# Optimization experiments

Hardware: AMD Instinct MI355X
Metric: run time of the kernel (lower is better)

Reference implementation:

```python
import jax, jax.numpy as jnp
import numpy as np

INPUT_DIM = 1024
EMBED_DIMS = 128


def setup_inputs() -> dict:
    key = jax.random.key(0)
    ks = jax.random.split(key, 7)
    s_in = 1.0 / np.sqrt(INPUT_DIM)
    x = jax.random.normal(ks[0], (4, 4096, INPUT_DIM), dtype=jnp.float32)
    Wq = jax.random.uniform(ks[1], (INPUT_DIM, EMBED_DIMS), jnp.float32, -s_in, s_in)
    bq = jax.random.uniform(ks[2], (EMBED_DIMS,), jnp.float32, -s_in, s_in)
    Wk = jax.random.uniform(ks[3], (INPUT_DIM, EMBED_DIMS), jnp.float32, -s_in, s_in)
    bk = jax.random.uniform(ks[4], (EMBED_DIMS,), jnp.float32, -s_in, s_in)
    Wv = jax.random.uniform(ks[5], (INPUT_DIM, EMBED_DIMS), jnp.float32, -s_in, s_in)
    bv = jax.random.uniform(ks[6], (EMBED_DIMS,), jnp.float32, -s_in, s_in)
    return {"x": x, "Wq": Wq, "bq": bq, "Wk": Wk, "bk": bk, "Wv": Wv, "bv": bv}


def reference(x, Wq, bq, Wk, bk, Wv, bv):
    # x: [B, L, C]
    Q = jnp.einsum('blc,cd->bld', x, Wq) + bq  # [B, L, D]
    K = jnp.einsum('blc,cd->bld', x, Wk) + bk
    V = jnp.einsum('blc,cd->bld', x, Wv) + bv
    d_k = Q.shape[-1]
    scores = jnp.einsum('bld,bmd->blm', Q, K) / jnp.sqrt(jnp.float32(d_k))  # [B, L, L]
    attn = jax.nn.softmax(scores, axis=-1)
    return jnp.einsum('blm,bmd->bld', attn, V)  # [B, L, D]
```

## Files before the change

### kernel.cpp

```cpp
#include <hip/hip_runtime.h>
#include <stdint.h>

typedef __bf16 bf16;
typedef __bf16 bf16x8 __attribute__((ext_vector_type(8)));
typedef __bf16 bf16x4 __attribute__((ext_vector_type(4)));
typedef _Float16 f16;
typedef f16 f16x8 __attribute__((ext_vector_type(8)));
typedef f16 f16x4 __attribute__((ext_vector_type(4)));
typedef float f32x4 __attribute__((ext_vector_type(4)));

#define LQ    16384
#define CDIM  1024
#define DDIM  128
#define NSPLIT 4
#define QS 0.12751741f

__global__ void prep_kernel(const float* __restrict__ Wq, const float* __restrict__ Wk,
                            const float* __restrict__ Wv, const float* __restrict__ bq,
                            const float* __restrict__ bk, const float* __restrict__ bv,
                            bf16* __restrict__ Wt, float* __restrict__ bias_all) {
  int idx = blockIdx.x * 256 + threadIdx.x;
  int p = idx >> 17;
  int rem = idx & 131071;
  int k = rem >> 7, n = rem & 127;
  const float* W = (p == 0) ? Wq : (p == 1) ? Wk : Wv;
  float s = (p == 0) ? QS : 1.0f;
  Wt[(size_t)(p * 128 + n) * CDIM + k] = (bf16)(W[rem] * s);
  if (idx < 384) {
    int pp = idx >> 7, nn = idx & 127;
    const float* b = (pp == 0) ? bq : (pp == 1) ? bk : bv;
    bias_all[idx] = b[nn] * ((pp == 0) ? QS : 1.0f);
  }
}

__global__ __launch_bounds__(256, 2) void qkv_gemm(
    const float* __restrict__ x, const bf16* __restrict__ Wt,
    const float* __restrict__ bias_all,
    bf16* __restrict__ Qw, bf16* __restrict__ Kw, f16* __restrict__ Vtw) {
  __shared__ bf16 Al[128 * 72];
  __shared__ bf16 Bl[128 * 72];
  const int t = threadIdx.x;
  const int w = t >> 6;
  const int lane = t & 63;
  const int l15 = lane & 15;
  const int quad = lane >> 4;
  const int y = blockIdx.y;
  const int m0 = blockIdx.x * 128;
  const bf16* W = Wt + (size_t)y * (DDIM * CDIM);
  const int m_off = (w & 1) * 64;
  const int n_off = (w >> 1) * 64;

  f32x4 zero4 = {0.f, 0.f, 0.f, 0.f};
  f32x4 acc[4][4];
#pragma unroll
  for (int i = 0; i < 4; i++)
#pragma unroll
    for (int j = 0; j < 4; j++) acc[i][j] = zero4;

  const int xr[8] = { (0*256+t)>>4, (1*256+t)>>4, (2*256+t)>>4, (3*256+t)>>4,
                      (4*256+t)>>4, (5*256+t)>>4, (6*256+t)>>4, (7*256+t)>>4 };
  const int xc = (t & 15) << 2;
  const int wr = t >> 3;
  const int wc = (t & 7) << 3;

  float4 xa[8];
  bf16x8 wa[4];
#pragma unroll
  for (int c = 0; c < 8; c++)
    xa[c] = *(const float4*)&x[(size_t)(m0 + xr[c]) * CDIM + xc];
#pragma unroll
  for (int c = 0; c < 4; c++)
    wa[c] = *(const bf16x8*)&W[(size_t)(c * 32 + wr) * CDIM + wc];

  for (int kc = 0; kc < 16; kc++) {
    __syncthreads();
#pragma unroll
    for (int c = 0; c < 8; c++) {
      bf16x4 v;
      v[0] = (bf16)xa[c].x; v[1] = (bf16)xa[c].y;
      v[2] = (bf16)xa[c].z; v[3] = (bf16)xa[c].w;
      *(bf16x4*)&Al[xr[c] * 72 + xc] = v;
    }
#pragma unroll
    for (int c = 0; c < 4; c++)
      *(bf16x8*)&Bl[(c * 32 + wr) * 72 + wc] = wa[c];
    __syncthreads();

    const int kn = (kc < 15 ? kc + 1 : 15) * 64;
#pragma unroll
    for (int c = 0; c < 8; c++)
      xa[c] = *(const float4*)&x[(size_t)(m0 + xr[c]) * CDIM + kn + xc];
#pragma unroll
    for (int c = 0; c < 4; c++)
      wa[c] = *(const bf16x8*)&W[(size_t)(c * 32 + wr) * CDIM + kn + wc];

#pragma unroll
    for (int ks = 0; ks < 2; ks++) {
      bf16x8 af[4], bfr[4];
#pragma unroll
      for (int mt = 0; mt < 4; mt++)
        af[mt] = *(const bf16x8*)&Al[(m_off + mt * 16 + l15) * 72 + ks * 32 + quad * 8];
#pragma unroll
      for (int nt = 0; nt < 4; nt++)
        bfr[nt] = *(const bf16x8*)&Bl[(n_off + nt * 16 + l15) * 72 + ks * 32 + quad * 8];
#pragma unroll
      for (int mt = 0; mt < 4; mt++)
#pragma unroll
        for (int nt = 0; nt < 4; nt++)
          acc[mt][nt] = __builtin_amdgcn_mfma_f32_16x16x32_bf16(af[mt], bfr[nt], acc[mt][nt], 0, 0, 0);
    }
  }

  float bias4[4];
#pragma unroll
  for (int nt = 0; nt < 4; nt++) bias4[nt] = bias_all[y * 128 + n_off + nt * 16 + l15];

  if (y < 2) {
    bf16* outp = (y == 0) ? Qw : Kw;
#pragma unroll
    for (int mt = 0; mt < 4; mt++)
#pragma unroll
      for (int nt = 0; nt < 4; nt++) {
        int n = n_off + nt * 16 + l15;
#pragma unroll
        for (int r = 0; r < 4; r++) {
          int m = m0 + m_off + mt * 16 + quad * 4 + r;
          outp[(size_t)m * DDIM + n] = (bf16)(acc[mt][nt][r] + bias4[nt]);
        }
      }
  } else {
#pragma unroll
    for (int mt = 0; mt < 4; mt++)
#pragma unroll
      for (int nt = 0; nt < 4; nt++) {
        int n = n_off + nt * 16 + l15;
        int m = m0 + m_off + mt * 16 + quad * 4;
        f16x4 pv;
#pragma unroll
        for (int r = 0; r < 4; r++) pv[r] = (f16)(acc[mt][nt][r] + bias4[nt]);
        *(f16x4*)&Vtw[(size_t)n * LQ + m] = pv;
      }
  }
}

__global__ __launch_bounds__(128, 2) void flash_kernel(
    const bf16* __restrict__ Qw, const bf16* __restrict__ Kw, const f16* __restrict__ Vtw,
    bf16* __restrict__ Opb, float* __restrict__ lp) {
  __shared__ bf16 Kl[64 * 136];
  __shared__ f16  Vl[128 * 72];

  const int t = threadIdx.x;
  const int w = t >> 6;
  const int lane = t & 63;
  const int l15 = lane & 15;
  const int quad = lane >> 4;
  const int qb = blockIdx.x;
  const int sp = blockIdx.y;
  const int batch = qb >> 6;
  const int q0w = qb * 64 + w * 32;
  const int kv_base = batch * 4096 + sp * 1024;

  bf16x8 qf[2][4];
#pragma unroll
  for (int nq = 0; nq < 2; nq++)
#pragma unroll
    for (int ks = 0; ks < 4; ks++)
      qf[nq][ks] = *(const bf16x8*)&Qw[(size_t)(q0w + nq * 16 + l15) * DDIM + ks * 32 + quad * 8];

  f32x4 zero4 = {0.f, 0.f, 0.f, 0.f};
  f32x4 o[2][8];
#pragma unroll
  for (int nq = 0; nq < 2; nq++)
#pragma unroll
    for (int dt = 0; dt < 8; dt++) o[nq][dt] = zero4;
  f32x4 li4[2];
  li4[0] = zero4; li4[1] = zero4;

  f16x4 onef = {(f16)1.f, (f16)1.f, (f16)1.f, (f16)1.f};

  const int kr = t >> 4;
  const int kcol = (t & 15) << 3;
  const int vr = t >> 3;
  const int vcol = (t & 7) << 3;

  bf16x8 ka[8];
  f16x8 va[8];
#pragma unroll
  for (int c = 0; c < 8; c++)
    ka[c] = *(const bf16x8*)&Kw[(size_t)(kv_base + c * 8 + kr) * DDIM + kcol];
#pragma unroll
  for (int c = 0; c < 8; c++)
    va[c] = *(const f16x8*)&Vtw[(size_t)(c * 16 + vr) * LQ + kv_base + vcol];

  for (int tile = 0; tile < 16; tile++) {
    __syncthreads();
#pragma unroll
    for (int c = 0; c < 8; c++)
      *(bf16x8*)&Kl[(c * 8 + kr) * 136 + kcol] = ka[c];
#pragma unroll
    for (int c = 0; c < 8; c++)
      *(f16x8*)&Vl[(c * 16 + vr) * 72 + vcol] = va[c];
    __syncthreads();

    const int kvn = kv_base + (tile < 15 ? tile + 1 : 15) * 64;
#pragma unroll
    for (int c = 0; c < 8; c++)
      ka[c] = *(const bf16x8*)&Kw[(size_t)(kvn + c * 8 + kr) * DDIM + kcol];
#pragma unroll
    for (int c = 0; c < 8; c++)
      va[c] = *(const f16x8*)&Vtw[(size_t)(c * 16 + vr) * LQ + kvn + vcol];

    f32x4 sv[4][2];
#pragma unroll
    for (int mk = 0; mk < 4; mk++)
#pragma unroll
      for (int nq = 0; nq < 2; nq++) sv[mk][nq] = zero4;
#pragma unroll
    for (int ks = 0; ks < 4; ks++) {
      bf16x8 kf[4];
#pragma unroll
      for (int mk = 0; mk < 4; mk++)
        kf[mk] = *(const bf16x8*)&Kl[(mk * 16 + l15) * 136 + ks * 32 + quad * 8];
#pragma unroll
      for (int mk = 0; mk < 4; mk++)
#pragma unroll
        for (int nq = 0; nq < 2; nq++)
          sv[mk][nq] = __builtin_amdgcn_mfma_f32_16x16x32_bf16(kf[mk], qf[nq][ks], sv[mk][nq], 0, 0, 0);
    }

#pragma unroll
    for (int mk = 0; mk < 4; mk++)
#pragma unroll
      for (int nq = 0; nq < 2; nq++)
#pragma unroll
        for (int r = 0; r < 4; r++)
          sv[mk][nq][r] = exp2f(sv[mk][nq][r]);

#pragma unroll
    for (int s = 0; s < 4; s++) {
      f16x4 pa[2];
#pragma unroll
      for (int nq = 0; nq < 2; nq++) {
        f16x4 p;
#pragma unroll
        for (int r = 0; r < 4; r++) p[r] = (f16)sv[s][nq][r];
        pa[nq] = p;
      }
#pragma unroll
      for (int dt = 0; dt < 8; dt++) {
        f16x4 vf = *(const f16x4*)&Vl[(dt * 16 + l15) * 72 + s * 16 + quad * 4];
#pragma unroll
        for (int nq = 0; nq < 2; nq++)
          o[nq][dt] = __builtin_amdgcn_mfma_f32_16x16x16f16(pa[nq], vf, o[nq][dt], 0, 0, 0);
      }
#pragma unroll
      for (int nq = 0; nq < 2; nq++)
        li4[nq] = __builtin_amdgcn_mfma_f32_16x16x16f16(pa[nq], onef, li4[nq], 0, 0, 0);
    }
  }

  const size_t po = (size_t)sp * LQ * DDIM;
#pragma unroll
  for (int nq = 0; nq < 2; nq++)
#pragma unroll
    for (int dt = 0; dt < 8; dt++)
#pragma unroll
      for (int r = 0; r < 4; r++)
        Opb[po + (size_t)(q0w + nq * 16 + quad * 4 + r) * DDIM + dt * 16 + l15] = (bf16)o[nq][dt][r];
  if (l15 == 0) {
#pragma unroll
    for (int nq = 0; nq < 2; nq++)
#pragma unroll
      for (int r = 0; r < 4; r++)
        lp[(size_t)sp * LQ + q0w + nq * 16 + quad * 4 + r] = li4[nq][r];
  }
}

__global__ void combine_kernel(const bf16* __restrict__ Opb, const float* __restrict__ lp,
                               float* __restrict__ out) {
  int idx = blockIdx.x * 256 + threadIdx.x;
  int q = idx >> 5;
  int d = (idx & 31) * 4;
  float lsum = 0.f;
  float acc[4] = {0.f, 0.f, 0.f, 0.f};
#pragma unroll
  for (int sp = 0; sp < NSPLIT; sp++) {
    lsum += lp[(size_t)sp * LQ + q];
    bf16x4 ov = *(const bf16x4*)&Opb[(size_t)sp * LQ * DDIM + (size_t)q * DDIM + d];
#pragma unroll
    for (int j = 0; j < 4; j++) acc[j] += (float)ov[j];
  }
  float inv = 1.0f / lsum;
  float4 r;
  r.x = acc[0] * inv; r.y = acc[1] * inv; r.z = acc[2] * inv; r.w = acc[3] * inv;
  *(float4*)&out[(size_t)q * DDIM + d] = r;
}

extern "C" void kernel_launch(void* const* d_in, const int* in_sizes, int n_in,
                              void* d_out, int out_size, void* d_ws, size_t ws_size,
                              hipStream_t stream) {
  const float* x  = (const float*)d_in[0];
  const float* Wq = (const float*)d_in[1];
  const float* bq = (const float*)d_in[2];
  const float* Wk = (const float*)d_in[3];
  const float* bk = (const float*)d_in[4];
  const float* Wv = (const float*)d_in[5];
  const float* bv = (const float*)d_in[6];
  char* ws = (char*)d_ws;
  bf16* Qw   = (bf16*)(ws);
  bf16* Kw   = (bf16*)(ws + ((size_t)4 << 20));
  f16*  Vtw  = (f16*)(ws + ((size_t)8 << 20));
  bf16* Wt   = (bf16*)(ws + ((size_t)12 << 20));
  float* bias_all = (float*)(ws + ((size_t)12 << 20) + 786432);
  bf16* Opb  = (bf16*)(ws + ((size_t)13 << 20));
  float* lpp = (float*)(ws + ((size_t)29 << 20));
  float* out = (float*)d_out;

  prep_kernel<<<1536, 256, 0, stream>>>(Wq, Wk, Wv, bq, bk, bv, Wt, bias_all);
  qkv_gemm<<<dim3(128, 3), 256, 0, stream>>>(x, Wt, bias_all, Qw, Kw, Vtw);
  flash_kernel<<<dim3(256, NSPLIT), 128, 0, stream>>>(Qw, Kw, Vtw, Opb, lpp);
  combine_kernel<<<2048, 256, 0, stream>>>(Opb, lpp, out);
}
```

Before: 185.8 us.

## Double-buffer LDS tiles in QKV GEMM and flash kernel, widen flash blocks

Both the projection GEMM and the attention kernel now ping-pong between two LDS buffers, dropping one barrier per iteration so global loads for the next tile are issued before the single sync. The flash kernel is relaunched with 256 threads covering 128 query rows per block, so each K/V tile staged in LDS is shared by four waves instead of two. This halves the K/V global traffic per query but doubles LDS usage per block and halves the grid size, which may affect occupancy.

```diff
diff --git a/kernel.cpp b/kernel.cpp
--- a/kernel.cpp
+++ b/kernel.cpp
@@ -37,8 +37,8 @@
     const float* __restrict__ x, const bf16* __restrict__ Wt,
     const float* __restrict__ bias_all,
     bf16* __restrict__ Qw, bf16* __restrict__ Kw, f16* __restrict__ Vtw) {
-  __shared__ bf16 Al[128 * 72];
-  __shared__ bf16 Bl[128 * 72];
+  __shared__ bf16 Al[2][128 * 72];
+  __shared__ bf16 Bl[2][128 * 72];
   const int t = threadIdx.x;
   const int w = t >> 6;
   const int lane = t & 63;
@@ -57,8 +57,7 @@
 #pragma unroll
     for (int j = 0; j < 4; j++) acc[i][j] = zero4;
 
-  const int xr[8] = { (0*256+t)>>4, (1*256+t)>>4, (2*256+t)>>4, (3*256+t)>>4,
-                      (4*256+t)>>4, (5*256+t)>>4, (6*256+t)>>4, (7*256+t)>>4 };
+  const int xrr = t >> 4;
   const int xc = (t & 15) << 2;
   const int wr = t >> 3;
   const int wc = (t & 7) << 3;
@@ -67,42 +66,44 @@
   bf16x8 wa[4];
 #pragma unroll
   for (int c = 0; c < 8; c++)
-    xa[c] = *(const float4*)&x[(size_t)(m0 + xr[c]) * CDIM + xc];
+    xa[c] = *(const float4*)&x[(size_t)(m0 + c * 16 + xrr) * CDIM + xc];
 #pragma unroll
   for (int c = 0; c < 4; c++)
     wa[c] = *(const bf16x8*)&W[(size_t)(c * 32 + wr) * CDIM + wc];
 
   for (int kc = 0; kc < 16; kc++) {
-    __syncthreads();
+    bf16* Ab = Al[kc & 1];
+    bf16* Bb = Bl[kc & 1];
 #pragma unroll
     for (int c = 0; c < 8; c++) {
       bf16x4 v;
       v[0] = (bf16)xa[c].x; v[1] = (bf16)xa[c].y;
       v[2] = (bf16)xa[c].z; v[3] = (bf16)xa[c].w;
-      *(bf16x4*)&Al[xr[c] * 72 + xc] = v;
+      *(bf16x4*)&Ab[(c * 16 + xrr) * 72 + xc] = v;
     }
 #pragma unroll
     for (int c = 0; c < 4; c++)
-      *(bf16x8*)&Bl[(c * 32 + wr) * 72 + wc] = wa[c];
+      *(bf16x8*)&Bb[(c * 32 + wr) * 72 + wc] = wa[c];
+
+    const int kn = (kc < 15 ? kc + 1 : 15) * 64;
+#pragma unroll
+    for (int c = 0; c < 8; c++)
+      xa[c] = *(const float4*)&x[(size_t)(m0 + c * 16 + xrr) * CDIM + kn + xc];
+#pragma unroll
+    for (int c = 0; c < 4; c++)
+      wa[c] = *(const bf16x8*)&W[(size_t)(c * 32 + wr) * CDIM + kn + wc];
+
     __syncthreads();
-
-    const int kn = (kc < 15 ? kc + 1 : 15) * 64;
-#pragma unroll
-    for (int c = 0; c < 8; c++)
-      xa[c] = *(const float4*)&x[(size_t)(m0 + xr[c]) * CDIM + kn + xc];
-#pragma unroll
-    for (int c = 0; c < 4; c++)
-      wa[c] = *(const bf16x8*)&W[(size_t)(c * 32 + wr) * CDIM + kn + wc];
 
 #pragma unroll
     for (int ks = 0; ks < 2; ks++) {
       bf16x8 af[4], bfr[4];
 #pragma unroll
       for (int mt = 0; mt < 4; mt++)
-        af[mt] = *(const bf16x8*)&Al[(m_off + mt * 16 + l15) * 72 + ks * 32 + quad * 8];
+        af[mt] = *(const bf16x8*)&Ab[(m_off + mt * 16 + l15) * 72 + ks * 32 + quad * 8];
 #pragma unroll
       for (int nt = 0; nt < 4; nt++)
-        bfr[nt] = *(const bf16x8*)&Bl[(n_off + nt * 16 + l15) * 72 + ks * 32 + quad * 8];
+        bfr[nt] = *(const bf16x8*)&Bb[(n_off + nt * 16 + l15) * 72 + ks * 32 + quad * 8];
 #pragma unroll
       for (int mt = 0; mt < 4; mt++)
 #pragma unroll
@@ -143,11 +144,11 @@
   }
 }
 
-__global__ __launch_bounds__(128, 2) void flash_kernel(
+__global__ __launch_bounds__(256, 2) void flash_kernel(
     const bf16* __restrict__ Qw, const bf16* __restrict__ Kw, const f16* __restrict__ Vtw,
     bf16* __restrict__ Opb, float* __restrict__ lp) {
-  __shared__ bf16 Kl[64 * 136];
-  __shared__ f16  Vl[128 * 72];
+  __shared__ bf16 Kl[2][64 * 136];
+  __shared__ f16  Vl[2][128 * 72];
 
   const int t = threadIdx.x;
   const int w = t >> 6;
@@ -156,8 +157,8 @@
   const int quad = lane >> 4;
   const int qb = blockIdx.x;
   const int sp = blockIdx.y;
-  const int batch = qb >> 6;
-  const int q0w = qb * 64 + w * 32;
+  const int batch = qb >> 5;
+  const int q0w = qb * 128 + w * 32;
   const int kv_base = batch * 4096 + sp * 1024;
 
   bf16x8 qf[2][4];
@@ -183,32 +184,34 @@
   const int vr = t >> 3;
   const int vcol = (t & 7) << 3;
 
-  bf16x8 ka[8];
-  f16x8 va[8];
-#pragma unroll
-  for (int c = 0; c < 8; c++)
-    ka[c] = *(const bf16x8*)&Kw[(size_t)(kv_base + c * 8 + kr) * DDIM + kcol];
-#pragma unroll
-  for (int c = 0; c < 8; c++)
-    va[c] = *(const f16x8*)&Vtw[(size_t)(c * 16 + vr) * LQ + kv_base + vcol];
+  bf16x8 ka[4];
+  f16x8 va[4];
+#pragma unroll
+  for (int c = 0; c < 4; c++)
+    ka[c] = *(const bf16x8*)&Kw[(size_t)(kv_base + c * 16 + kr) * DDIM + kcol];
+#pragma unroll
+  for (int c = 0; c < 4; c++)
+    va[c] = *(const f16x8*)&Vtw[(size_t)(c * 32 + vr) * LQ + kv_base + vcol];
 
   for (int tile = 0; tile < 16; tile++) {
+    bf16* Kb = Kl[tile & 1];
+    f16*  Vb = Vl[tile & 1];
+#pragma unroll
+    for (int c = 0; c < 4; c++)
+      *(bf16x8*)&Kb[(c * 16 + kr) * 136 + kcol] = ka[c];
+#pragma unroll
+    for (int c = 0; c < 4; c++)
+      *(f16x8*)&Vb[(c * 32 + vr) * 72 + vcol] = va[c];
+
+    const int kvn = kv_base + (tile < 15 ? tile + 1 : 15) * 64;
+#pragma unroll
+    for (int c = 0; c < 4; c++)
+      ka[c] = *(const bf16x8*)&Kw[(size_t)(kvn + c * 16 + kr) * DDIM + kcol];
+#pragma unroll
+    for (int c = 0; c < 4; c++)
+      va[c] = *(const f16x8*)&Vtw[(size_t)(c * 32 + vr) * LQ + kvn + vcol];
+
     __syncthreads();
-#pragma unroll
-    for (int c = 0; c < 8; c++)
-      *(bf16x8*)&Kl[(c * 8 + kr) * 136 + kcol] = ka[c];
-#pragma unroll
-    for (int c = 0; c < 8; c++)
-      *(f16x8*)&Vl[(c * 16 + vr) * 72 + vcol] = va[c];
-    __syncthreads();
-
-    const int kvn = kv_base + (tile < 15 ? tile + 1 : 15) * 64;
-#pragma unroll
-    for (int c = 0; c < 8; c++)
-      ka[c] = *(const bf16x8*)&Kw[(size_t)(kvn + c * 8 + kr) * DDIM + kcol];
-#pragma unroll
-    for (int c = 0; c < 8; c++)
-      va[c] = *(const f16x8*)&Vtw[(size_t)(c * 16 + vr) * LQ + kvn + vcol];
 
     f32x4 sv[4][2];
 #pragma unroll
@@ -220,7 +223,7 @@
       bf16x8 kf[4];
 #pragma unroll
       for (int mk = 0; mk < 4; mk++)
-        kf[mk] = *(const bf16x8*)&Kl[(mk * 16 + l15) * 136 + ks * 32 + quad * 8];
+        kf[mk] = *(const bf16x8*)&Kb[(mk * 16 + l15) * 136 + ks * 32 + quad * 8];
 #pragma unroll
       for (int mk = 0; mk < 4; mk++)
 #pragma unroll
@@ -248,7 +251,7 @@
       }
 #pragma unroll
       for (int dt = 0; dt < 8; dt++) {
-        f16x4 vf = *(const f16x4*)&Vl[(dt * 16 + l15) * 72 + s * 16 + quad * 4];
+        f16x4 vf = *(const f16x4*)&Vb[(dt * 16 + l15) * 72 + s * 16 + quad * 4];
 #pragma unroll
         for (int nq = 0; nq < 2; nq++)
           o[nq][dt] = __builtin_amdgcn_mfma_f32_16x16x16f16(pa[nq], vf, o[nq][dt], 0, 0, 0);
@@ -318,6 +321,6 @@
 
   prep_kernel<<<1536, 256, 0, stream>>>(Wq, Wk, Wv, bq, bk, bv, Wt, bias_all);
   qkv_gemm<<<dim3(128, 3), 256, 0, stream>>>(x, Wt, bias_all, Qw, Kw, Vtw);
-  flash_kernel<<<dim3(256, NSPLIT), 128, 0, stream>>>(Qw, Kw, Vtw, Opb, lpp);
+  flash_kernel<<<dim3(128, NSPLIT), 256, 0, stream>>>(Qw, Kw, Vtw, Opb, lpp);
   combine_kernel<<<2048, 256, 0, stream>>>(Opb, lpp, out);
 }
```

Result: no change. 182.8 us (-1.6%).
